# Kernel optimization log

Measured on AMD Instinct MI355X. Metric: run time of the kernel, lower is better.

## Reference

```python
import jax, jax.numpy as jnp
import numpy as np

B, D, C = 4096, 2048, 64
L_HP, D_HP, OMEGA, EPSILON = 0.5, 1.0, 100.0, 0.1
LN_EPS = 1e-5
CLASS_COUNTS = [5000,4500,4050,3645,3280,2952,2657,2391,2152,1937,1743,1569,1412,1271,1144,1029,926,834,750,675,608,547,492,443,399,359,323,291,262,236,212,191,172,155,139,125,113,101,91,82,74,66,60,54,48,43,39,35,32,28,26,23,21,19,17,15,14,12,11,10,9,8,7,7]


def setup_inputs() -> dict:
    key = jax.random.key(0)
    k_x, k_y, k_b, k_u1, k_u2 = jax.random.split(key, 5)
    counts = jnp.asarray(CLASS_COUNTS, dtype=jnp.float32)
    # set_class_weights: tilde_C = 1/log(counts*d + eps), min-max normalized, scaled by l
    tilde = 1.0 / jnp.log(counts * D_HP + EPSILON)
    c = (tilde - jnp.min(tilde)) / (jnp.max(tilde) - jnp.min(tilde)) * L_HP
    # set_fs_classes: 1 where count <= omega
    fs_classes = jnp.where(counts <= OMEGA, 1, 0).astype(jnp.int32)
    x = jax.random.normal(k_x, (B, D), dtype=jnp.float32)
    y = jax.random.randint(k_y, (B,), 0, C)
    beta_idx = jax.random.randint(k_b, (B,), 0, B)
    u1 = jax.random.uniform(k_u1, (B,))
    u2 = jax.random.uniform(k_u2, (B,))
    alpha = jnp.where(u1 > 0.5, u2, jnp.ones((B,), jnp.float32))
    return {"x": x, "y": y, "alpha": alpha, "beta_idx": beta_idx, "c": c, "fs_classes": fs_classes}


def reference(x, y, alpha, beta_idx, c, fs_classes):
    n_batch, dim = x.shape
    num_classes = c.shape[0]
    # --- reconstruct ---
    mu = jnp.mean(x, axis=-1, keepdims=True)
    var = jnp.mean((x - mu) ** 2, axis=-1, keepdims=True)
    x_norm = (x - mu) / jnp.sqrt(var + LN_EPS) / jnp.sqrt(jnp.asarray(dim, x.dtype))
    sim = jnp.matmul(x_norm, x_norm.T)  # [B, B]
    # E[i, j] = eye[i, j] + fs_mask[j]  (broadcast over rows), thresholded to {0, 1}
    fs_mask = fs_classes[y].astype(x.dtype)  # [B]
    E = jnp.eye(n_batch, dtype=x.dtype) + fs_mask[None, :]
    E = jnp.where(E >= 1.0, 1.0, 0.0)
    sim = jax.nn.softmax(sim - 100000.0 * E, axis=-1)
    contrib = c[y]  # [B]
    reconstructions = jnp.matmul(sim, x)  # [B, D]
    R = reconstructions * contrib[:, None] + x * (1.0 - contrib)[:, None]
    # --- pairwise_mix: M @ R with M[i,:] = alpha[i]*e_i + (1-alpha[i])*e_{beta_idx[i]} ---
    y_oh = jax.nn.one_hot(y, num_classes, dtype=x.dtype)
    a = alpha[:, None]
    x_mix = a * R + (1.0 - a) * R[beta_idx]
    y_mix = a * y_oh + (1.0 - a) * y_oh[beta_idx]
    return (x_mix, y_mix)
```

## Files before the change

kernel.cpp:

```cpp
#include <hip/hip_runtime.h>
#include <cstdint>
#include <cstddef>

typedef __bf16 bf16;
typedef __bf16 bf16x8 __attribute__((ext_vector_type(8)));
typedef float floatx4 __attribute__((ext_vector_type(4)));
typedef int intx8 __attribute__((ext_vector_type(8)));

#define NB 4096
#define ND 2048
#define NCLS 64
#define TS 80
#define OS 72

__device__ __forceinline__ void stage16(const void* g, void* l) {
  __builtin_amdgcn_global_load_lds(
      (__attribute__((address_space(1))) unsigned int*)g,
      (__attribute__((address_space(3))) unsigned int*)l, 16, 0, 0);
}

__device__ __forceinline__ unsigned char fp8x1(float f) {
  return (unsigned char)(__builtin_amdgcn_cvt_pk_fp8_f32(f, f, 0, false) & 0xFF);
}
__device__ __forceinline__ int fp8x4(float f0, float f1, float f2, float f3) {
  int d = __builtin_amdgcn_cvt_pk_fp8_f32(f0, f1, 0, false);
  return __builtin_amdgcn_cvt_pk_fp8_f32(f2, f3, d, true);
}

__device__ __forceinline__ void gemm_core64(
    const unsigned char* __restrict__ Abase, const int aoff[4],
    const unsigned char* __restrict__ Bbase, const int boff[2], int nk,
    unsigned char* __restrict__ As0, unsigned char* __restrict__ Bs0,
    unsigned char* __restrict__ As1, unsigned char* __restrict__ Bs1,
    floatx4 acc[2][4], int w, int lane) {
  const int lm = lane & 15, quad = lane >> 4;
  auto STAGE = [&](int k0, unsigned char* As, unsigned char* Bs) {
#pragma unroll
    for (int q = 0; q < 4; ++q)
      stage16(Abase + (size_t)(aoff[q] + k0), As + w * 4096 + q * 1024);
#pragma unroll
    for (int q = 0; q < 2; ++q)
      stage16(Bbase + (size_t)(boff[q] + k0), Bs + w * 2048 + q * 1024);
  };
  STAGE(0, As0, Bs0);
  for (int k = 0; k < nk; ++k) {
    __syncthreads();
    if (k + 1 < nk)
      STAGE((k + 1) << 7, (k & 1) ? As0 : As1, (k & 1) ? Bs0 : Bs1);
    const unsigned char* Ac = (k & 1) ? As1 : As0;
    const unsigned char* Bc = (k & 1) ? Bs1 : Bs0;

    intx8 af[2], bf[4];
#pragma unroll
    for (int i = 0; i < 2; ++i) {
      const int row = w * 32 + i * 16 + lm;
      const int c0 = (quad * 2) ^ (row & 7);
      const int4 lo = *(const int4*)(Ac + row * 128 + c0 * 16);
      const int4 hi = *(const int4*)(Ac + row * 128 + (c0 ^ 1) * 16);
      af[i][0] = lo.x; af[i][1] = lo.y; af[i][2] = lo.z; af[i][3] = lo.w;
      af[i][4] = hi.x; af[i][5] = hi.y; af[i][6] = hi.z; af[i][7] = hi.w;
    }
#pragma unroll
    for (int i = 0; i < 4; ++i) {
      const int row = i * 16 + lm;
      const int c0 = (quad * 2) ^ (row & 7);
      const int4 lo = *(const int4*)(Bc + row * 128 + c0 * 16);
      const int4 hi = *(const int4*)(Bc + row * 128 + (c0 ^ 1) * 16);
      bf[i][0] = lo.x; bf[i][1] = lo.y; bf[i][2] = lo.z; bf[i][3] = lo.w;
      bf[i][4] = hi.x; bf[i][5] = hi.y; bf[i][6] = hi.z; bf[i][7] = hi.w;
    }
#pragma unroll
    for (int mi = 0; mi < 2; ++mi)
#pragma unroll
      for (int ni = 0; ni < 4; ++ni)
        acc[mi][ni] = __builtin_amdgcn_mfma_scale_f32_16x16x128_f8f6f4(
            af[mi], bf[ni], acc[mi][ni], 0, 0, 0, 127, 0, 127);
  }
}


__global__ __launch_bounds__(1024) void perm_kernel(
    const int* __restrict__ y, const int* __restrict__ fs,
    const float* __restrict__ c, int* __restrict__ perm,
    int* __restrict__ minfo, float* __restrict__ lrow,
    float* __restrict__ contrib) {
  const int t = threadIdx.x;
  const int base = t * 4;
  int fl[4];
  int cnt = 0;
#pragma unroll
  for (int j = 0; j < 4; ++j) {
    const int yi = y[base + j];
    fl[j] = (fs[yi] == 0) ? 1 : 0;
    cnt += fl[j];
    contrib[base + j] = c[yi];
    lrow[base + j] = 0.0f;
  }
  const int lane = t & 63, w = t >> 6;
  int inc = cnt;
#pragma unroll
  for (int o = 1; o < 64; o <<= 1) {
    int v = __shfl_up(inc, o);
    if (lane >= o) inc += v;
  }
  __shared__ int wsum[16];
  __shared__ int Msh;
  if (lane == 63) wsum[w] = inc;
  __syncthreads();
  int wbase = 0;
  for (int i = 0; i < w; ++i) wbase += wsum[i];
  int pos = wbase + inc - cnt;
#pragma unroll
  for (int j = 0; j < 4; ++j)
    if (fl[j]) perm[pos++] = base + j;
  if (t == 1023) Msh = wbase + inc;
  __syncthreads();
  const int M = Msh;
  const int Mp = (M + 127) & ~127;
  if (t < Mp - M) perm[M + t] = 0;
  if (t == 0) {
    minfo[0] = M;
    minfo[1] = Mp;
    minfo[2] = Mp >> 7;
  }
}

__global__ __launch_bounds__(256) void prep_kernel(
    const float* __restrict__ x, unsigned char* __restrict__ XN8,
    unsigned char* __restrict__ XBT8, const int* __restrict__ perm,
    const int* __restrict__ minfo) {
  __shared__ float tile[64][65];
  const int t = threadIdx.x;

  if (blockIdx.x < NB) {
    const int row = blockIdx.x;
    const float4* xr = (const float4*)(x + (size_t)row * ND);
    float4 v0 = xr[t], v1 = xr[t + 256];
    float s = v0.x + v0.y + v0.z + v0.w + v1.x + v1.y + v1.z + v1.w;
    float q = v0.x * v0.x + v0.y * v0.y + v0.z * v0.z + v0.w * v0.w +
              v1.x * v1.x + v1.y * v1.y + v1.z * v1.z + v1.w * v1.w;
#pragma unroll
    for (int o = 32; o > 0; o >>= 1) {
      s += __shfl_down(s, o);
      q += __shfl_down(q, o);
    }
    const int w = t >> 6;
    if ((t & 63) == 0) { tile[0][w] = s; tile[1][w] = q; }
    __syncthreads();
    s = tile[0][0] + tile[0][1] + tile[0][2] + tile[0][3];
    q = tile[1][0] + tile[1][1] + tile[1][2] + tile[1][3];
    const float mu = s * (1.0f / ND);
    const float var = q * (1.0f / ND) - mu * mu;
    const float sc =
        rsqrtf(var + 1e-5f) * 0.02209708691207961f * 32.0f;

    int* orow = (int*)(XN8 + (size_t)row * ND);
    orow[t] = fp8x4((v0.x - mu) * sc, (v0.y - mu) * sc, (v0.z - mu) * sc,
                    (v0.w - mu) * sc);
    orow[256 + t] = fp8x4((v1.x - mu) * sc, (v1.y - mu) * sc, (v1.z - mu) * sc,
                          (v1.w - mu) * sc);
  } else {
    const int b2 = blockIdx.x - NB;
    const int rb = b2 & 63;
    const int cb = b2 >> 6;
    if (rb * 64 >= minfo[1]) return;
    const int tx = t & 63, ty = t >> 6;
#pragma unroll
    for (int rr = ty; rr < 64; rr += 4)
      tile[rr][tx] = x[(size_t)perm[rb * 64 + rr] * ND + cb * 64 + tx];
    __syncthreads();
    const int ro = t >> 2;
    const int co = t & 3;
    int4 v;
    {
      const int j = co * 16;
      v.x = fp8x4(tile[j + 0][ro], tile[j + 1][ro], tile[j + 2][ro], tile[j + 3][ro]);
      v.y = fp8x4(tile[j + 4][ro], tile[j + 5][ro], tile[j + 6][ro], tile[j + 7][ro]);
      v.z = fp8x4(tile[j + 8][ro], tile[j + 9][ro], tile[j + 10][ro], tile[j + 11][ro]);
      v.w = fp8x4(tile[j + 12][ro], tile[j + 13][ro], tile[j + 14][ro], tile[j + 15][ro]);
    }
    *(int4*)(XBT8 + (size_t)(cb * 64 + ro) * NB + rb * 64 + co * 16) = v;
  }
}

__global__ __launch_bounds__(256, 3) void gemm_sim_kernel(
    const unsigned char* __restrict__ XN8, unsigned char* __restrict__ P8,
    float* __restrict__ lrow, const int* __restrict__ perm,
    const int* __restrict__ minfo) {
  __shared__ unsigned char smem[49152];
  unsigned char* As0 = smem;
  unsigned char* As1 = smem + 16384;
  unsigned char* Bs0 = smem + 32768;
  unsigned char* Bs1 = smem + 40960;

  const int Mp = minfo[1];
  const int id = blockIdx.x;
  const int xcd = id & 7;
  const int s = id >> 3;
  const int bi = xcd * 4 + (s & 3);
  const int bjc = s >> 2;
  const int n0 = bjc * 64;
  if (n0 >= Mp) return;
  const int M = minfo[0];
  const int m0 = bi * 128;

  const int t = threadIdx.x, w = t >> 6, lane = t & 63;
  const int lm = lane & 15, quad = lane >> 4;

  int aoff[4], boff[2];
#pragma unroll
  for (int q = 0; q < 4; ++q) {
    const int slot = w * 256 + q * 64 + lane;
    const int row = slot >> 3;
    const int cc = (slot & 7) ^ (row & 7);
    aoff[q] = (m0 + row) * ND + cc * 16;
  }
#pragma unroll
  for (int q = 0; q < 2; ++q) {
    const int slot = w * 128 + q * 64 + lane;
    const int row = slot >> 3;
    const int cc = (slot & 7) ^ (row & 7);
    boff[q] = perm[n0 + row] * ND + cc * 16;
  }

  floatx4 acc[2][4];
#pragma unroll
  for (int i = 0; i < 2; ++i)
#pragma unroll
    for (int j = 0; j < 4; ++j) acc[i][j] = 0.0f;

  gemm_core64(XN8, aoff, XN8, boff, ND >> 7, As0, Bs0, As1, Bs1, acc, w, lane);

  int pcol[4], valid[4];
#pragma unroll
  for (int ni = 0; ni < 4; ++ni) {
    const int gc = n0 + ni * 16 + lm;
    valid[ni] = (gc < M) ? 1 : 0;
    pcol[ni] = perm[gc];
  }

  float rs[2][4];
#pragma unroll
  for (int mi = 0; mi < 2; ++mi)
#pragma unroll
    for (int r = 0; r < 4; ++r) rs[mi][r] = 0.0f;

#pragma unroll
  for (int ni = 0; ni < 4; ++ni) {
#pragma unroll
    for (int mi = 0; mi < 2; ++mi) {
#pragma unroll
      for (int r = 0; r < 4; ++r) {
        const int grow = m0 + w * 32 + mi * 16 + quad * 4 + r;
        const float e = (valid[ni] && grow != pcol[ni])
                            ? __expf(acc[mi][ni][r] * 0.0009765625f)
                            : 0.0f;
        acc[mi][ni][r] = e;
        rs[mi][r] += e;
      }
    }
  }
#pragma unroll
  for (int mi = 0; mi < 2; ++mi)
#pragma unroll
    for (int r = 0; r < 4; ++r) {
      float vsum = rs[mi][r];
      vsum += __shfl_xor(vsum, 1);
      vsum += __shfl_xor(vsum, 2);
      vsum += __shfl_xor(vsum, 4);
      vsum += __shfl_xor(vsum, 8);
      if (lm == 0)
        atomicAdd(&lrow[m0 + w * 32 + mi * 16 + quad * 4 + r], vsum);
    }

  __syncthreads();
#pragma unroll
  for (int ni = 0; ni < 4; ++ni) {
    const int col = ni * 16 + lm;
#pragma unroll
    for (int mi = 0; mi < 2; ++mi)
#pragma unroll
      for (int r = 0; r < 4; ++r) {
        const int row = w * 32 + mi * 16 + quad * 4 + r;
        smem[row * TS + col] = fp8x1(acc[mi][ni][r]);
      }
  }
  __syncthreads();
#pragma unroll
  for (int it = 0; it < 2; ++it) {
    const int row = it * 64 + (t >> 2), ch = t & 3;
    int4 v = *(const int4*)(smem + row * TS + ch * 16);
    *(int4*)(P8 + (size_t)(m0 + row) * NB + n0 + ch * 16) = v;
  }
}

__global__ __launch_bounds__(256, 3) void gemm_recon_kernel(
    const unsigned char* __restrict__ P8, const unsigned char* __restrict__ XBT8,
    const float* __restrict__ x, const float* __restrict__ lrow,
    const float* __restrict__ contrib, const int* __restrict__ minfo,
    bf16* __restrict__ R) {
  __shared__ unsigned char smem[49152];
  unsigned char* As0 = smem;
  unsigned char* As1 = smem + 16384;
  unsigned char* Bs0 = smem + 32768;
  unsigned char* Bs1 = smem + 40960;

  const int id = blockIdx.x;
  const int xcd = id & 7;
  const int s = id >> 3;
  const int by = xcd * 4 + (s & 3);
  const int bx = s >> 2;
  const int m0 = by * 128, n0 = bx * 64;

  const int t = threadIdx.x, w = t >> 6, lane = t & 63;
  const int lm = lane & 15, quad = lane >> 4;

  int aoff[4], boff[2];
#pragma unroll
  for (int q = 0; q < 4; ++q) {
    const int slot = w * 256 + q * 64 + lane;
    const int row = slot >> 3;
    const int cc = (slot & 7) ^ (row & 7);
    aoff[q] = (m0 + row) * NB + cc * 16;
  }
#pragma unroll
  for (int q = 0; q < 2; ++q) {
    const int slot = w * 128 + q * 64 + lane;
    const int row = slot >> 3;
    const int cc = (slot & 7) ^ (row & 7);
    boff[q] = (n0 + row) * NB + cc * 16;
  }

  floatx4 acc[2][4];
#pragma unroll
  for (int i = 0; i < 2; ++i)
#pragma unroll
    for (int j = 0; j < 4; ++j) acc[i][j] = 0.0f;

  gemm_core64(P8, aoff, XBT8, boff, minfo[2], As0, Bs0, As1, Bs1, acc, w,
              lane);

  __syncthreads();
  bf16* osm = (bf16*)smem;
#pragma unroll
  for (int mi = 0; mi < 2; ++mi) {
#pragma unroll
    for (int r = 0; r < 4; ++r) {
      const int lrow_i = w * 32 + mi * 16 + quad * 4 + r;
      const int grow = m0 + lrow_i;
      const float inv = 1.0f / lrow[grow];
      const float ci = contrib[grow];
#pragma unroll
      for (int ni = 0; ni < 4; ++ni) {
        const int lcol = ni * 16 + lm;
        const float rec = acc[mi][ni][r] * inv;
        const float xv = x[(size_t)grow * ND + n0 + lcol];
        osm[lrow_i * OS + lcol] = (bf16)(rec * ci + xv * (1.0f - ci));
      }
    }
  }
  __syncthreads();
#pragma unroll
  for (int it = 0; it < 4; ++it) {
    const int row = it * 32 + (t >> 3), ch = t & 7;
    int4 v = *(const int4*)(osm + row * OS + ch * 8);
    *(int4*)(R + (size_t)(m0 + row) * ND + n0 + ch * 8) = v;
  }
}

__global__ __launch_bounds__(256) void mix_kernel(
    const bf16* __restrict__ R, const float* __restrict__ alpha,
    const int* __restrict__ beta_idx, const int* __restrict__ y,
    float* __restrict__ out) {
  const int i = blockIdx.x, t = threadIdx.x;
  const float a = alpha[i];
  const int bi = beta_idx[i];
  const bf16x8* Ri = (const bf16x8*)(R + (size_t)i * ND);
  const bf16x8* Rb = (const bf16x8*)(R + (size_t)bi * ND);
  const float b = 1.0f - a;
  bf16x8 r = Ri[t], g = Rb[t];
  float4 o0, o1;
  o0.x = a * (float)r[0] + b * (float)g[0];
  o0.y = a * (float)r[1] + b * (float)g[1];
  o0.z = a * (float)r[2] + b * (float)g[2];
  o0.w = a * (float)r[3] + b * (float)g[3];
  o1.x = a * (float)r[4] + b * (float)g[4];
  o1.y = a * (float)r[5] + b * (float)g[5];
  o1.z = a * (float)r[6] + b * (float)g[6];
  o1.w = a * (float)r[7] + b * (float)g[7];
  float4* o = (float4*)(out + (size_t)i * ND + t * 8);
  o[0] = o0;
  o[1] = o1;
  if (t < NCLS) {
    const int yi = y[i], yb = y[bi];
    const float v = a * (t == yi ? 1.0f : 0.0f) + b * (t == yb ? 1.0f : 0.0f);
    out[(size_t)NB * ND + (size_t)i * NCLS + t] = v;
  }
}

extern "C" void kernel_launch(void* const* d_in, const int* in_sizes, int n_in,
                              void* d_out, int out_size, void* d_ws,
                              size_t ws_size, hipStream_t stream) {
  const float* x = (const float*)d_in[0];
  const int* y = (const int*)d_in[1];
  const float* alpha = (const float*)d_in[2];
  const int* beta = (const int*)d_in[3];
  const float* c = (const float*)d_in[4];
  const int* fs = (const int*)d_in[5];
  float* out = (float*)d_out;
  char* ws = (char*)d_ws;

  unsigned char* XN8  = (unsigned char*)(ws + 0);
  unsigned char* XBT8 = (unsigned char*)(ws + 8388608);
  unsigned char* P8   = (unsigned char*)(ws + 16777216);
  bf16* R   = (bf16*)(ws + 33554432);
  float* LR = (float*)(ws + 50331648);
  float* CT = (float*)(ws + 50331648 + 16384);
  int* PERM = (int*)(ws + 50331648 + 32768);
  int* MINFO = (int*)(ws + 50331648 + 49152);

  perm_kernel<<<1, 1024, 0, stream>>>(y, fs, c, PERM, MINFO, LR, CT);
  prep_kernel<<<NB + 2048, 256, 0, stream>>>(x, XN8, XBT8, PERM, MINFO);
  gemm_sim_kernel<<<1280, 256, 0, stream>>>(XN8, P8, LR, PERM, MINFO);
  gemm_recon_kernel<<<1024, 256, 0, stream>>>(P8, XBT8, x, LR, CT, MINFO, R);
  mix_kernel<<<NB, 256, 0, stream>>>(R, alpha, beta, y, out);
}
```

Measured before the change: 170.4 us.

## Prefetch B tiles into registers two steps ahead with manual waitcnt

Restructures the GEMM main loop so B-operand tiles are loaded into registers several k-steps ahead and then written to LDS, while A continues to use direct global-to-LDS staging. Explicit s_waitcnt counters and raw s_barrier replace __syncthreads to keep more memory operations in flight. This aims to hide global load latency for the B operand. In exchange it adds register pressure, relies on hand-counted vmcnt values that could become wrong, and the lane*16 LDS write layout must match what stage16 produced.

```diff
diff --git a/kernel.cpp b/kernel.cpp
--- a/kernel.cpp
+++ b/kernel.cpp
@@ -34,21 +34,45 @@
     unsigned char* __restrict__ As1, unsigned char* __restrict__ Bs1,
     floatx4 acc[2][4], int w, int lane) {
   const int lm = lane & 15, quad = lane >> 4;
-  auto STAGE = [&](int k0, unsigned char* As, unsigned char* Bs) {
+  const int aw = w * 4096;
+  const int bw = w * 2048;
+
+  auto STAGE_A = [&](int k0, unsigned char* As) {
 #pragma unroll
     for (int q = 0; q < 4; ++q)
-      stage16(Abase + (size_t)(aoff[q] + k0), As + w * 4096 + q * 1024);
+      stage16(Abase + (size_t)(aoff[q] + k0), As + aw + q * 1024);
+  };
+  auto STAGE_B_LDS = [&](int k0, unsigned char* Bs) {
 #pragma unroll
     for (int q = 0; q < 2; ++q)
-      stage16(Bbase + (size_t)(boff[q] + k0), Bs + w * 2048 + q * 1024);
+      stage16(Bbase + (size_t)(boff[q] + k0), Bs + bw + q * 1024);
   };
-  STAGE(0, As0, Bs0);
-  for (int k = 0; k < nk; ++k) {
-    __syncthreads();
-    if (k + 1 < nk)
-      STAGE((k + 1) << 7, (k & 1) ? As0 : As1, (k & 1) ? Bs0 : Bs1);
-    const unsigned char* Ac = (k & 1) ? As1 : As0;
-    const unsigned char* Bc = (k & 1) ? Bs1 : Bs0;
+  int4 bregA[2], bregB[2];
+  auto GLOADB = [&](int k0, int4 br[2]) {
+#pragma unroll
+    for (int q = 0; q < 2; ++q)
+      br[q] = *(const int4*)(Bbase + (size_t)(boff[q] + k0));
+  };
+  auto DSWB = [&](unsigned char* Bs, const int4 br[2]) {
+#pragma unroll
+    for (int q = 0; q < 2; ++q)
+      *(int4*)(Bs + bw + q * 1024 + lane * 16) = br[q];
+  };
+
+  auto STEP = [&](int k, const unsigned char* Ac, const unsigned char* Bc,
+                  unsigned char* An, unsigned char* Bn, int4 br[2]) {
+    if (k == 0)
+      asm volatile("s_waitcnt vmcnt(4) lgkmcnt(0)" ::: "memory");
+    else if (k + 2 < nk)
+      asm volatile("s_waitcnt vmcnt(2) lgkmcnt(0)" ::: "memory");
+    else
+      asm volatile("s_waitcnt vmcnt(0) lgkmcnt(0)" ::: "memory");
+    __builtin_amdgcn_s_barrier();
+    if (k + 1 < nk) {
+      DSWB(Bn, br);
+      STAGE_A((k + 1) << 7, An);
+    }
+    if (k + 3 < nk) GLOADB((k + 3) << 7, br);
 
     intx8 af[2], bf[4];
 #pragma unroll
@@ -75,6 +99,20 @@
       for (int ni = 0; ni < 4; ++ni)
         acc[mi][ni] = __builtin_amdgcn_mfma_scale_f32_16x16x128_f8f6f4(
             af[mi], bf[ni], acc[mi][ni], 0, 0, 0, 127, 0, 127);
+  };
+
+  STAGE_A(0, As0);
+  STAGE_B_LDS(0, Bs0);
+  GLOADB(1 << 7, bregA);
+  GLOADB(2 << 7, bregB);
+
+  int k = 0;
+  while (k < nk) {
+    STEP(k, As0, Bs0, As1, Bs1, bregA);
+    ++k;
+    if (k >= nk) break;
+    STEP(k, As1, Bs1, As0, Bs0, bregB);
+    ++k;
   }
 }
 
```

After: 230.3 us. 1.35x slower.

## Prefetch B tiles into registers two stages ahead in GEMM core loop

Applied to the files above, without the earlier changes.

Rewrites the shared FP8 GEMM main loop so B tiles are loaded into registers three k-steps ahead and written to LDS manually, while A tiles keep the async global-to-LDS path. The __syncthreads is replaced by explicit vmcnt/lgkmcnt waits plus s_barrier, with sched_barriers pinning instruction order. The aim is to hide global load latency behind more in-flight requests. It costs extra VGPRs, and the hand-written waitcnt counts must match the issued loads exactly.

```diff
diff --git a/kernel.cpp b/kernel.cpp
--- a/kernel.cpp
+++ b/kernel.cpp
@@ -29,53 +29,93 @@
 
 __device__ __forceinline__ void gemm_core64(
     const unsigned char* __restrict__ Abase, const int aoff[4],
-    const unsigned char* __restrict__ Bbase, const int boff[2], int nk,
+    const unsigned char* __restrict__ Bbase, int boff0, int boff1, int nk,
     unsigned char* __restrict__ As0, unsigned char* __restrict__ Bs0,
     unsigned char* __restrict__ As1, unsigned char* __restrict__ Bs1,
     floatx4 acc[2][4], int w, int lane) {
   const int lm = lane & 15, quad = lane >> 4;
-  auto STAGE = [&](int k0, unsigned char* As, unsigned char* Bs) {
-#pragma unroll
-    for (int q = 0; q < 4; ++q)
-      stage16(Abase + (size_t)(aoff[q] + k0), As + w * 4096 + q * 1024);
-#pragma unroll
-    for (int q = 0; q < 2; ++q)
-      stage16(Bbase + (size_t)(boff[q] + k0), Bs + w * 2048 + q * 1024);
-  };
-  STAGE(0, As0, Bs0);
-  for (int k = 0; k < nk; ++k) {
-    __syncthreads();
-    if (k + 1 < nk)
-      STAGE((k + 1) << 7, (k & 1) ? As0 : As1, (k & 1) ? Bs0 : Bs1);
-    const unsigned char* Ac = (k & 1) ? As1 : As0;
-    const unsigned char* Bc = (k & 1) ? Bs1 : Bs0;
-
-    intx8 af[2], bf[4];
-#pragma unroll
-    for (int i = 0; i < 2; ++i) {
-      const int row = w * 32 + i * 16 + lm;
-      const int c0 = (quad * 2) ^ (row & 7);
-      const int4 lo = *(const int4*)(Ac + row * 128 + c0 * 16);
-      const int4 hi = *(const int4*)(Ac + row * 128 + (c0 ^ 1) * 16);
-      af[i][0] = lo.x; af[i][1] = lo.y; af[i][2] = lo.z; af[i][3] = lo.w;
-      af[i][4] = hi.x; af[i][5] = hi.y; af[i][6] = hi.z; af[i][7] = hi.w;
-    }
-#pragma unroll
-    for (int i = 0; i < 4; ++i) {
-      const int row = i * 16 + lm;
-      const int c0 = (quad * 2) ^ (row & 7);
-      const int4 lo = *(const int4*)(Bc + row * 128 + c0 * 16);
-      const int4 hi = *(const int4*)(Bc + row * 128 + (c0 ^ 1) * 16);
-      bf[i][0] = lo.x; bf[i][1] = lo.y; bf[i][2] = lo.z; bf[i][3] = lo.w;
-      bf[i][4] = hi.x; bf[i][5] = hi.y; bf[i][6] = hi.z; bf[i][7] = hi.w;
-    }
-#pragma unroll
-    for (int mi = 0; mi < 2; ++mi)
-#pragma unroll
-      for (int ni = 0; ni < 4; ++ni)
-        acc[mi][ni] = __builtin_amdgcn_mfma_scale_f32_16x16x128_f8f6f4(
-            af[mi], bf[ni], acc[mi][ni], 0, 0, 0, 127, 0, 127);
-  }
+  const int aw = w * 4096;
+  const int bw = w * 2048;
+
+#define STAGE_A_(k0, As)                                               \
+  do {                                                                 \
+    stage16(Abase + (size_t)(aoff[0] + (k0)), (As) + aw);              \
+    stage16(Abase + (size_t)(aoff[1] + (k0)), (As) + aw + 1024);       \
+    stage16(Abase + (size_t)(aoff[2] + (k0)), (As) + aw + 2048);       \
+    stage16(Abase + (size_t)(aoff[3] + (k0)), (As) + aw + 3072);       \
+  } while (0)
+
+  int4 pb0, pb1, qb0, qb1;
+
+  STAGE_A_(0, As0);
+  stage16(Bbase + (size_t)boff0, Bs0 + bw);
+  stage16(Bbase + (size_t)boff1, Bs0 + bw + 1024);
+  __builtin_amdgcn_sched_barrier(0);
+  pb0 = *(const int4*)(Bbase + (size_t)(boff0 + 128));
+  pb1 = *(const int4*)(Bbase + (size_t)(boff1 + 128));
+  __builtin_amdgcn_sched_barrier(0);
+  qb0 = *(const int4*)(Bbase + (size_t)(boff0 + 256));
+  qb1 = *(const int4*)(Bbase + (size_t)(boff1 + 256));
+  __builtin_amdgcn_sched_barrier(0);
+
+#define STEP_(kk, Ac, Bc, An, Bn, B0, B1)                               \
+  do {                                                                  \
+    if ((kk) + 2 < nk)                                                  \
+      asm volatile("s_waitcnt vmcnt(2) lgkmcnt(0)" ::: "memory");       \
+    else                                                                \
+      asm volatile("s_waitcnt vmcnt(0) lgkmcnt(0)" ::: "memory");       \
+    __builtin_amdgcn_sched_barrier(0);                                  \
+    __builtin_amdgcn_s_barrier();                                       \
+    __builtin_amdgcn_sched_barrier(0);                                  \
+    if ((kk) + 1 < nk) {                                                \
+      *(int4*)((Bn) + bw + lane * 16) = B0;                             \
+      *(int4*)((Bn) + bw + 1024 + lane * 16) = B1;                      \
+      STAGE_A_(((kk) + 1) << 7, An);                                    \
+    }                                                                   \
+    __builtin_amdgcn_sched_barrier(0);                                  \
+    if ((kk) + 3 < nk) {                                                \
+      B0 = *(const int4*)(Bbase + (size_t)(boff0 + (((kk) + 3) << 7))); \
+      B1 = *(const int4*)(Bbase + (size_t)(boff1 + (((kk) + 3) << 7))); \
+    }                                                                   \
+    __builtin_amdgcn_sched_barrier(0);                                  \
+    intx8 af[2], bf[4];                                                 \
+    _Pragma("unroll")                                                   \
+    for (int i = 0; i < 2; ++i) {                                       \
+      const int row = w * 32 + i * 16 + lm;                             \
+      const int c0 = (quad * 2) ^ (row & 7);                            \
+      const int4 lo = *(const int4*)((Ac) + row * 128 + c0 * 16);       \
+      const int4 hi = *(const int4*)((Ac) + row * 128 + (c0 ^ 1) * 16); \
+      af[i][0] = lo.x; af[i][1] = lo.y; af[i][2] = lo.z;                \
+      af[i][3] = lo.w; af[i][4] = hi.x; af[i][5] = hi.y;                \
+      af[i][6] = hi.z; af[i][7] = hi.w;                                 \
+    }                                                                   \
+    _Pragma("unroll")                                                   \
+    for (int i = 0; i < 4; ++i) {                                       \
+      const int row = i * 16 + lm;                                      \
+      const int c0 = (quad * 2) ^ (row & 7);                            \
+      const int4 lo = *(const int4*)((Bc) + row * 128 + c0 * 16);       \
+      const int4 hi = *(const int4*)((Bc) + row * 128 + (c0 ^ 1) * 16); \
+      bf[i][0] = lo.x; bf[i][1] = lo.y; bf[i][2] = lo.z;                \
+      bf[i][3] = lo.w; bf[i][4] = hi.x; bf[i][5] = hi.y;                \
+      bf[i][6] = hi.z; bf[i][7] = hi.w;                                 \
+    }                                                                   \
+    _Pragma("unroll")                                                   \
+    for (int mi = 0; mi < 2; ++mi)                                      \
+      _Pragma("unroll")                                                 \
+      for (int ni = 0; ni < 4; ++ni)                                    \
+        acc[mi][ni] = __builtin_amdgcn_mfma_scale_f32_16x16x128_f8f6f4( \
+            af[mi], bf[ni], acc[mi][ni], 0, 0, 0, 127, 0, 127);         \
+  } while (0)
+
+  int k = 0;
+  while (true) {
+    STEP_(k, As0, Bs0, As1, Bs1, pb0, pb1);
+    if (++k >= nk) break;
+    STEP_(k, As1, Bs1, As0, Bs0, qb0, qb1);
+    if (++k >= nk) break;
+  }
+#undef STEP_
+#undef STAGE_A_
 }
 
 
@@ -207,7 +247,7 @@
   const int t = threadIdx.x, w = t >> 6, lane = t & 63;
   const int lm = lane & 15, quad = lane >> 4;
 
-  int aoff[4], boff[2];
+  int aoff[4];
 #pragma unroll
   for (int q = 0; q < 4; ++q) {
     const int slot = w * 256 + q * 64 + lane;
@@ -215,12 +255,14 @@
     const int cc = (slot & 7) ^ (row & 7);
     aoff[q] = (m0 + row) * ND + cc * 16;
   }
-#pragma unroll
-  for (int q = 0; q < 2; ++q) {
-    const int slot = w * 128 + q * 64 + lane;
-    const int row = slot >> 3;
-    const int cc = (slot & 7) ^ (row & 7);
-    boff[q] = perm[n0 + row] * ND + cc * 16;
+  int boff0, boff1;
+  {
+    const int slot0 = w * 128 + lane;
+    const int row0 = slot0 >> 3;
+    boff0 = perm[n0 + row0] * ND + ((slot0 & 7) ^ (row0 & 7)) * 16;
+    const int slot1 = w * 128 + 64 + lane;
+    const int row1 = slot1 >> 3;
+    boff1 = perm[n0 + row1] * ND + ((slot1 & 7) ^ (row1 & 7)) * 16;
   }
 
   floatx4 acc[2][4];
@@ -229,7 +271,8 @@
 #pragma unroll
     for (int j = 0; j < 4; ++j) acc[i][j] = 0.0f;
 
-  gemm_core64(XN8, aoff, XN8, boff, ND >> 7, As0, Bs0, As1, Bs1, acc, w, lane);
+  gemm_core64(XN8, aoff, XN8, boff0, boff1, ND >> 7, As0, Bs0, As1, Bs1, acc,
+              w, lane);
 
   int pcol[4], valid[4];
 #pragma unroll
@@ -315,7 +358,7 @@
   const int t = threadIdx.x, w = t >> 6, lane = t & 63;
   const int lm = lane & 15, quad = lane >> 4;
 
-  int aoff[4], boff[2];
+  int aoff[4];
 #pragma unroll
   for (int q = 0; q < 4; ++q) {
     const int slot = w * 256 + q * 64 + lane;
@@ -323,12 +366,14 @@
     const int cc = (slot & 7) ^ (row & 7);
     aoff[q] = (m0 + row) * NB + cc * 16;
   }
-#pragma unroll
-  for (int q = 0; q < 2; ++q) {
-    const int slot = w * 128 + q * 64 + lane;
-    const int row = slot >> 3;
-    const int cc = (slot & 7) ^ (row & 7);
-    boff[q] = (n0 + row) * NB + cc * 16;
+  int boff0, boff1;
+  {
+    const int slot0 = w * 128 + lane;
+    const int row0 = slot0 >> 3;
+    boff0 = (n0 + row0) * NB + ((slot0 & 7) ^ (row0 & 7)) * 16;
+    const int slot1 = w * 128 + 64 + lane;
+    const int row1 = slot1 >> 3;
+    boff1 = (n0 + row1) * NB + ((slot1 & 7) ^ (row1 & 7)) * 16;
   }
 
   floatx4 acc[2][4];
@@ -337,8 +382,8 @@
 #pragma unroll
     for (int j = 0; j < 4; ++j) acc[i][j] = 0.0f;
 
-  gemm_core64(P8, aoff, XBT8, boff, minfo[2], As0, Bs0, As1, Bs1, acc, w,
-              lane);
+  gemm_core64(P8, aoff, XBT8, boff0, boff1, minfo[2], As0, Bs0, As1, Bs1, acc,
+              w, lane);
 
   __syncthreads();
   bf16* osm = (bf16*)smem;
```

After: 184.4 us. +8.2%, slower.
